# Performance work log

Measured on AMD Instinct MI355X. Metric: run time of the kernel, lower is better.

## Reference

```python
import jax, jax.numpy as jnp
import numpy as np

BATCH, FIELD0, EMB = 1024, 32, 64
LAYER_SIZES = (128, 128, 128)  # split_half=True -> hidden field sizes [32, 64, 64]


def setup_inputs() -> dict:
    key = jax.random.key(0)
    ks = jax.random.split(key, 7)
    x = jax.random.normal(ks[0], (BATCH, FIELD0, EMB), dtype=jnp.float32)
    # Conv1D(kernel_size=1) weights: (in_channels=f0*fi, filters=layer_size), plus bias.
    field_sizes = [FIELD0]
    params = {}
    for i, size in enumerate(LAYER_SIZES):
        fi = field_sizes[-1]
        fan_in = FIELD0 * fi
        scale = 1.0 / np.sqrt(fan_in)
        params[f"W{i}"] = jax.random.normal(ks[1 + 2 * i], (fan_in, size), dtype=jnp.float32) * scale
        params[f"b{i}"] = jnp.zeros((size,), dtype=jnp.float32)
        field_sizes.append(size // 2 if i != len(LAYER_SIZES) - 1 else size)
    return {"x": x, **params}


def reference(x, W0, b0, W1, b1, W2, b2):
    # CIN: outer product + 1x1 conv (a matmul over the flattened field-pair axis)
    # fused as a single bilinear contraction per layer:
    #   cur[b,k,e] = sum_{i,j} x[b,i,e] * hidden[b,j,e] * W[i,j,k] + b[k]
    Ws = [(W0, b0), (W1, b1), (W2, b2)]
    f0 = x.shape[1]
    hidden = x
    final_outputs = []
    n_layers = len(Ws)
    for idx, (W, b) in enumerate(Ws):
        fi = hidden.shape[1]
        Wr = W.reshape(f0, fi, W.shape[-1])  # channel m = i*fi + j (row-major reshape)
        cur = jnp.einsum('bie,bje,ijk->bke', x, hidden, Wr) + b[None, :, None]
        # activation=None -> linear
        if idx != n_layers - 1:
            half = cur.shape[1] // 2
            hidden, direct = cur[:, :half, :], cur[:, half:, :]
        else:
            direct = cur
        final_outputs.append(direct)
    result = jnp.concatenate(final_outputs, axis=1)  # (B, 64+64+128, E)
    return jnp.sum(result, axis=-1)  # (B, 256)
```

## Files before the change

kernel.cpp:

```cpp
#include <hip/hip_runtime.h>
#include <cstdint>


typedef _Float16 half8  __attribute__((ext_vector_type(8)));
typedef _Float16 half4_ __attribute__((ext_vector_type(4)));
typedef _Float16 half2_ __attribute__((ext_vector_type(2)));
typedef float    f32x4  __attribute__((ext_vector_type(4)));

__global__ void pack_w_all(const float* __restrict__ W0, _Float16* __restrict__ Wt0,
                           const float* __restrict__ W1, _Float16* __restrict__ Wt1,
                           const float* __restrict__ W2, _Float16* __restrict__ Wt2)
{
    __shared__ _Float16 ldsT[128 * 33];
    const int blk = blockIdx.x, t = threadIdx.x;
    const float* W;
    _Float16* Wt;
    int c;
    if (blk < 32)       { W = W0; Wt = Wt0; c = blk; }
    else if (blk < 96)  { W = W1; Wt = Wt1; c = blk - 32; }
    else                { W = W2; Wt = Wt2; c = blk - 96; }

    for (int p = t; p < 32 * 128; p += 256) {
        int kk = p >> 7, m = p & 127;
        ldsT[m * 33 + kk] = (_Float16)W[(size_t)(c * 32 + kk) * 128 + m];
    }
    __syncthreads();
    int m = t >> 1, kk0 = (t & 1) * 16;
    half8 v0, v1;
#pragma unroll
    for (int i = 0; i < 8; ++i) {
        v0[i] = ldsT[m * 33 + kk0 + i];
        v1[i] = ldsT[m * 33 + kk0 + 8 + i];
    }
    *(half8*)(Wt + (size_t)c * 4096 + t * 16)     = v0;
    *(half8*)(Wt + (size_t)c * 4096 + t * 16 + 8) = v1;
}

template<int NCH, int ISH, int PH>
__device__ __forceinline__ void kloop_t(f32x4 (&acc)[2][4],
    const _Float16* __restrict__ WtL, const _Float16* __restrict__ hb,
    const _Float16* __restrict__ sX, int lr, int q, int ms, int kh)
{
#pragma unroll
    for (int mt = 0; mt < 2; ++mt)
#pragma unroll
        for (int nt = 0; nt < 4; ++nt)
            acc[mt][nt] = f32x4{0.0f, 0.0f, 0.0f, 0.0f};

    constexpr int HC = NCH / 2;
    const int c0 = kh * HC;
    const _Float16* aG = WtL + (size_t)c0 * 4096 + (ms * 32 + lr) * 32 + q * 8;
    const _Float16* hP = hb + lr * PH + q * 8;
    const _Float16* xP = sX + lr;

    half8 afA[2], afB[2], hvA[4], hvB[4];
    _Float16 xsA[4], xsB[4];

    auto pf = [&](half8* af, half8* hv, _Float16* xs, int cc) {
        const int c  = c0 + cc;
        const int i  = c >> ISH;
        const int j0 = (c & ((1 << ISH) - 1)) << 5;
        const _Float16* ag = aG + (size_t)cc * 4096;
        af[0] = *(const half8*)(ag);
        af[1] = *(const half8*)(ag + 512);
        const _Float16* hh = hP + j0;
        const _Float16* xb = xP + (i << 6);
#pragma unroll
        for (int nt = 0; nt < 4; ++nt) {
            hv[nt] = *(const half8*)(hh + nt * (PH * 16));
            xs[nt] = xb[nt * 16];
        }
    };
    auto cp = [&](half8* af, half8* hv, _Float16* xs) {
#pragma unroll
        for (int nt = 0; nt < 4; ++nt) {
            half2_ xv2 = {xs[nt], xs[nt]};
            half8 xv8 = __builtin_shufflevector(xv2, xv2, 0, 1, 0, 1, 0, 1, 0, 1);
            half8 bf = hv[nt] * xv8;
            acc[0][nt] = __builtin_amdgcn_mfma_f32_16x16x32_f16(
                af[0], bf, acc[0][nt], 0, 0, 0);
            acc[1][nt] = __builtin_amdgcn_mfma_f32_16x16x32_f16(
                af[1], bf, acc[1][nt], 0, 0, 0);
        }
    };

    pf(afA, hvA, xsA, 0);
    for (int cc = 0; cc < HC; cc += 2) {
        pf(afB, hvB, xsB, cc + 1);
        cp(afA, hvA, xsA);
        if (cc + 2 < HC) pf(afA, hvA, xsA, cc + 2);
        cp(afB, hvB, xsB);
    }
}

__global__ __launch_bounds__(256, 2)
void cin_fused(const float* __restrict__ x,
               const _Float16* __restrict__ Wt0,
               const _Float16* __restrict__ Wt1,
               const float* __restrict__ bs0,
               const float* __restrict__ bs1,
               _Float16* __restrict__ S0,
               _Float16* __restrict__ S1,
               _Float16* __restrict__ S2)
{
    __shared__ alignas(16) char smem[38912];
    _Float16* sX  = (_Float16*)smem;
    _Float16* R_A = (_Float16*)(smem + 4096);
    _Float16* R_B = (_Float16*)(smem + 13312);
    f32x4*    XC  = (f32x4*)   (smem + 22528);

    const int t = threadIdx.x, lane = t & 63, w = t >> 6;
    const int ms = w >> 1, kh = w & 1;
    const int lr = lane & 15, q = lane >> 4;
    const int b = blockIdx.x;

    {
        const float4* xv = (const float4*)(x + (size_t)b * 2048);
#pragma unroll
        for (int s = 0; s < 2; ++s) {
            int p4 = t + s * 256;
            float4 v = xv[p4];
            int idx = p4 * 4, i = idx >> 6, e0 = idx & 63;
            _Float16 h0 = (_Float16)v.x, h1 = (_Float16)v.y;
            _Float16 h2 = (_Float16)v.z, h3 = (_Float16)v.w;
            half4_ pk = {h0, h1, h2, h3};
            *(half4_*)(sX + i * 64 + e0) = pk;
            *(half4_*)(R_B + i * 72 + e0) = pk;
            R_A[(e0 + 0) * 40 + i] = h0;
            R_A[(e0 + 1) * 40 + i] = h1;
            R_A[(e0 + 2) * 40 + i] = h2;
            R_A[(e0 + 3) * 40 + i] = h3;
        }
    }
    __syncthreads();

    half8 aF[2][2];
#pragma unroll
    for (int it = 0; it < 2; ++it) {
        aF[it][0] = *(const half8*)(R_B + (it * 16 + lr) * 72 + q * 8);
        aF[it][1] = *(const half8*)(R_B + (it * 16 + lr) * 72 + q * 8 + 32);
    }

    f32x4 acc[2][4];

    const int wslot = ms * 2 + kh, pslot = ms * 2 + (1 - kh);
    auto xw = [&](const f32x4 (&a)[4]) {
#pragma unroll
        for (int nt = 0; nt < 4; ++nt)
            XC[wslot * 256 + nt * 64 + lane] = a[nt];
    };
    auto xr = [&](f32x4 (&a)[4]) {
#pragma unroll
        for (int nt = 0; nt < 4; ++nt)
            a[nt] += XC[pslot * 256 + nt * 64 + lane];
    };

    auto sgemm = [&](const _Float16* hJ, int fi, _Float16* Sdst) {
        const int nT = fi >> 3;
        for (int tt = w; tt < nT; tt += 4) {
            const int it = tt & 1, jt = tt >> 1;
            f32x4 sa = {0.0f, 0.0f, 0.0f, 0.0f};
            half8 bv0 = *(const half8*)(hJ + (jt * 16 + lr) * 72 + q * 8);
            half8 bv1 = *(const half8*)(hJ + (jt * 16 + lr) * 72 + q * 8 + 32);
            sa = __builtin_amdgcn_mfma_f32_16x16x32_f16(aF[it][0], bv0, sa, 0, 0, 0);
            sa = __builtin_amdgcn_mfma_f32_16x16x32_f16(aF[it][1], bv1, sa, 0, 0, 0);
#pragma unroll
            for (int r = 0; r < 4; ++r)
                Sdst[(size_t)b * (32 * fi) + (it * 16 + q * 4 + r) * fi
                     + jt * 16 + lr] = (_Float16)sa[r];
        }
    };

    auto epi_rows = [&](const f32x4 (&a)[4], const float* bs,
                        _Float16* hJ, _Float16* hT, bool wantT) {
        const int jb = ms * 32 + kh * 16 + q * 4;
        const float b0f = bs[jb + 0], b1f = bs[jb + 1];
        const float b2f = bs[jb + 2], b3f = bs[jb + 3];
#pragma unroll
        for (int nt = 0; nt < 4; ++nt) {
            const int e = nt * 16 + lr;
            half4_ vh;
            vh[0] = (_Float16)(a[nt][0] + b0f);
            vh[1] = (_Float16)(a[nt][1] + b1f);
            vh[2] = (_Float16)(a[nt][2] + b2f);
            vh[3] = (_Float16)(a[nt][3] + b3f);
            hJ[(jb + 0) * 72 + e] = vh[0];
            hJ[(jb + 1) * 72 + e] = vh[1];
            hJ[(jb + 2) * 72 + e] = vh[2];
            hJ[(jb + 3) * 72 + e] = vh[3];
            if (wantT) *(half4_*)(hT + e * 72 + jb) = vh;
        }
    };
    auto combine_epi = [&](const float* bs, _Float16* hJ, _Float16* hT,
                           bool wantT) {
        if (kh == 0) { xr(acc[0]); epi_rows(acc[0], bs, hJ, hT, wantT); }
        else         { xr(acc[1]); epi_rows(acc[1], bs, hJ, hT, wantT); }
    };

    sgemm(R_B, 32, S0);
    kloop_t<32, 0, 40>(acc, Wt0, R_A, sX, lr, q, ms, kh);
    if (kh == 0) xw(acc[1]); else xw(acc[0]);
    __syncthreads();
    combine_epi(bs0, R_A, R_B, true);
    __syncthreads();
    sgemm(R_A, 64, S1);
    kloop_t<64, 1, 72>(acc, Wt1, R_B, sX, lr, q, ms, kh);
    if (kh == 0) xw(acc[1]); else xw(acc[0]);
    __syncthreads();
    combine_epi(bs1, R_B, nullptr, false);
    __syncthreads();
    sgemm(R_B, 64, S2);
}

__global__ __launch_bounds__(256, 4)
void cin_direct(const _Float16* __restrict__ S0v, const _Float16* __restrict__ S1v,
                const _Float16* __restrict__ S2v,
                const _Float16* __restrict__ Wt0, const _Float16* __restrict__ Wt1,
                const _Float16* __restrict__ Wt2,
                const float* __restrict__ bs0, const float* __restrict__ bs1,
                const float* __restrict__ bs2,
                float* __restrict__ out)
{
    __shared__ f32x4 red[3][64];
    const int t = threadIdx.x, lane = t & 63, kh = t >> 6;
    const int lr = lane & 15, q = lane >> 4;
    const int task = blockIdx.x;

    const _Float16 *S, *Wt;
    const float* bias;
    int fan, nch, dm0, ob, idx;
    if (task < 256)      { S = S0v; Wt = Wt0; bias = bs0; fan = 1024; nch = 32; dm0 = 64; ob = 0;   idx = task; }
    else if (task < 512) { S = S1v; Wt = Wt1; bias = bs1; fan = 2048; nch = 64; dm0 = 64; ob = 64;  idx = task - 256; }
    else                 { S = S2v; Wt = Wt2; bias = bs2; fan = 2048; nch = 64; dm0 = 0;  ob = 128; idx = task - 512; }
    const int bt = idx & 63, kt = idx >> 6;
    const int bbase = bt * 16;
    const int hq = nch >> 2, c0 = kh * hq;

    const _Float16* aG = Wt + (size_t)(dm0 + kt * 16 + lr) * 32 + q * 8
                            + (size_t)c0 * 4096;
    const _Float16* bG = S + (size_t)(bbase + lr) * fan + q * 8 + c0 * 32;

    f32x4 acc = {0.0f, 0.0f, 0.0f, 0.0f};
    half8 aA = *(const half8*)(aG);
    half8 bA = *(const half8*)(bG);
    for (int c = 0; c < hq; c += 2) {
        half8 aB = *(const half8*)(aG + (size_t)(c + 1) * 4096);
        half8 bB = *(const half8*)(bG + (c + 1) * 32);
        acc = __builtin_amdgcn_mfma_f32_16x16x32_f16(aA, bA, acc, 0, 0, 0);
        if (c + 2 < hq) {
            aA = *(const half8*)(aG + (size_t)(c + 2) * 4096);
            bA = *(const half8*)(bG + (c + 2) * 32);
        }
        acc = __builtin_amdgcn_mfma_f32_16x16x32_f16(aB, bB, acc, 0, 0, 0);
    }
    if (kh != 0) red[kh - 1][lane] = acc;
    __syncthreads();
    if (kh == 0) {
#pragma unroll
        for (int p = 0; p < 3; ++p) {
            f32x4 o = red[p][lane];
#pragma unroll
            for (int r = 0; r < 4; ++r) acc[r] += o[r];
        }
#pragma unroll
        for (int r = 0; r < 4; ++r) {
            int kl = kt * 16 + q * 4 + r;
            out[(size_t)(bbase + lr) * 256 + ob + kl]
                = acc[r] + 64.0f * bias[dm0 + kl];
        }
    }
}

extern "C" void kernel_launch(void* const* d_in, const int* in_sizes, int n_in,
                              void* d_out, int out_size, void* d_ws, size_t ws_size,
                              hipStream_t stream)
{
    const float* x  = (const float*)d_in[0];
    const float* W0 = (const float*)d_in[1];
    const float* b0 = (const float*)d_in[2];
    const float* W1 = (const float*)d_in[3];
    const float* b1 = (const float*)d_in[4];
    const float* W2 = (const float*)d_in[5];
    const float* b2 = (const float*)d_in[6];
    float* out = (float*)d_out;

    char* ws = (char*)d_ws;
    _Float16* Wt0 = (_Float16*)(ws + 0);
    _Float16* Wt1 = (_Float16*)(ws + 262144);
    _Float16* Wt2 = (_Float16*)(ws + 786432);
    _Float16* S0  = (_Float16*)(ws + 1310720);
    _Float16* S1  = (_Float16*)(ws + 3407872);
    _Float16* S2  = (_Float16*)(ws + 7602176);
    (void)in_sizes; (void)n_in; (void)out_size; (void)ws_size;

    hipLaunchKernelGGL(pack_w_all, dim3(160), dim3(256), 0, stream,
                       W0, Wt0, W1, Wt1, W2, Wt2);

    hipLaunchKernelGGL(cin_fused, dim3(1024), dim3(256), 0, stream,
                       x, Wt0, Wt1, b0, b1, S0, S1, S2);

    hipLaunchKernelGGL(cin_direct, dim3(1024), dim3(256), 0, stream,
                       S0, S1, S2, Wt0, Wt1, Wt2, b0, b1, b2, out);
}
```

Baseline: 140.9 us.

## Split K four ways across waves and exchange partial sums in fp16 LDS

Result: faster. 115.5 us (-18.0%).

```diff
diff --git a/kernel.cpp b/kernel.cpp
--- a/kernel.cpp
+++ b/kernel.cpp
@@ -37,23 +37,23 @@
 }
 
 template<int NCH, int ISH, int PH>
-__device__ __forceinline__ void kloop_t(f32x4 (&acc)[2][4],
+__device__ __forceinline__ void kloop_t(f32x4 (&acc)[4][4],
     const _Float16* __restrict__ WtL, const _Float16* __restrict__ hb,
-    const _Float16* __restrict__ sX, int lr, int q, int ms, int kh)
-{
-#pragma unroll
-    for (int mt = 0; mt < 2; ++mt)
+    const _Float16* __restrict__ sX, int lr, int q, int w)
+{
+#pragma unroll
+    for (int mt = 0; mt < 4; ++mt)
 #pragma unroll
         for (int nt = 0; nt < 4; ++nt)
             acc[mt][nt] = f32x4{0.0f, 0.0f, 0.0f, 0.0f};
 
-    constexpr int HC = NCH / 2;
-    const int c0 = kh * HC;
-    const _Float16* aG = WtL + (size_t)c0 * 4096 + (ms * 32 + lr) * 32 + q * 8;
+    constexpr int HC = NCH / 4;
+    const int c0 = w * HC;
+    const _Float16* aG = WtL + (size_t)c0 * 4096 + lr * 32 + q * 8;
     const _Float16* hP = hb + lr * PH + q * 8;
     const _Float16* xP = sX + lr;
 
-    half8 afA[2], afB[2], hvA[4], hvB[4];
+    half8 afA[4], afB[4], hvA[4], hvB[4];
     _Float16 xsA[4], xsB[4];
 
     auto pf = [&](half8* af, half8* hv, _Float16* xs, int cc) {
@@ -61,8 +61,9 @@
         const int i  = c >> ISH;
         const int j0 = (c & ((1 << ISH) - 1)) << 5;
         const _Float16* ag = aG + (size_t)cc * 4096;
-        af[0] = *(const half8*)(ag);
-        af[1] = *(const half8*)(ag + 512);
+#pragma unroll
+        for (int mt = 0; mt < 4; ++mt)
+            af[mt] = *(const half8*)(ag + mt * 512);
         const _Float16* hh = hP + j0;
         const _Float16* xb = xP + (i << 6);
 #pragma unroll
@@ -77,10 +78,10 @@
             half2_ xv2 = {xs[nt], xs[nt]};
             half8 xv8 = __builtin_shufflevector(xv2, xv2, 0, 1, 0, 1, 0, 1, 0, 1);
             half8 bf = hv[nt] * xv8;
-            acc[0][nt] = __builtin_amdgcn_mfma_f32_16x16x32_f16(
-                af[0], bf, acc[0][nt], 0, 0, 0);
-            acc[1][nt] = __builtin_amdgcn_mfma_f32_16x16x32_f16(
-                af[1], bf, acc[1][nt], 0, 0, 0);
+#pragma unroll
+            for (int mt = 0; mt < 4; ++mt)
+                acc[mt][nt] = __builtin_amdgcn_mfma_f32_16x16x32_f16(
+                    af[mt], bf, acc[mt][nt], 0, 0, 0);
         }
     };
 
@@ -103,14 +104,13 @@
                _Float16* __restrict__ S1,
                _Float16* __restrict__ S2)
 {
-    __shared__ alignas(16) char smem[38912];
-    _Float16* sX  = (_Float16*)smem;
-    _Float16* R_A = (_Float16*)(smem + 4096);
-    _Float16* R_B = (_Float16*)(smem + 13312);
-    f32x4*    XC  = (f32x4*)   (smem + 22528);
+    __shared__ alignas(16) char smem[47104];
+    _Float16* sX   = (_Float16*)smem;
+    _Float16* R_A  = (_Float16*)(smem + 4096);
+    _Float16* R_B  = (_Float16*)(smem + 13312);
+    _Float16* XC16 = (_Float16*)(smem + 22528);
 
     const int t = threadIdx.x, lane = t & 63, w = t >> 6;
-    const int ms = w >> 1, kh = w & 1;
     const int lr = lane & 15, q = lane >> 4;
     const int b = blockIdx.x;
 
@@ -134,56 +134,56 @@
     }
     __syncthreads();
 
-    half8 aF[2][2];
-#pragma unroll
-    for (int it = 0; it < 2; ++it) {
-        aF[it][0] = *(const half8*)(R_B + (it * 16 + lr) * 72 + q * 8);
-        aF[it][1] = *(const half8*)(R_B + (it * 16 + lr) * 72 + q * 8 + 32);
-    }
-
-    f32x4 acc[2][4];
-
-    const int wslot = ms * 2 + kh, pslot = ms * 2 + (1 - kh);
-    auto xw = [&](const f32x4 (&a)[4]) {
-#pragma unroll
-        for (int nt = 0; nt < 4; ++nt)
-            XC[wslot * 256 + nt * 64 + lane] = a[nt];
-    };
-    auto xr = [&](f32x4 (&a)[4]) {
-#pragma unroll
-        for (int nt = 0; nt < 4; ++nt)
-            a[nt] += XC[pslot * 256 + nt * 64 + lane];
-    };
-
-    auto sgemm = [&](const _Float16* hJ, int fi, _Float16* Sdst) {
-        const int nT = fi >> 3;
-        for (int tt = w; tt < nT; tt += 4) {
-            const int it = tt & 1, jt = tt >> 1;
-            f32x4 sa = {0.0f, 0.0f, 0.0f, 0.0f};
-            half8 bv0 = *(const half8*)(hJ + (jt * 16 + lr) * 72 + q * 8);
-            half8 bv1 = *(const half8*)(hJ + (jt * 16 + lr) * 72 + q * 8 + 32);
-            sa = __builtin_amdgcn_mfma_f32_16x16x32_f16(aF[it][0], bv0, sa, 0, 0, 0);
-            sa = __builtin_amdgcn_mfma_f32_16x16x32_f16(aF[it][1], bv1, sa, 0, 0, 0);
-#pragma unroll
-            for (int r = 0; r < 4; ++r)
-                Sdst[(size_t)b * (32 * fi) + (it * 16 + q * 4 + r) * fi
-                     + jt * 16 + lr] = (_Float16)sa[r];
-        }
-    };
-
-    auto epi_rows = [&](const f32x4 (&a)[4], const float* bs,
-                        _Float16* hJ, _Float16* hT, bool wantT) {
-        const int jb = ms * 32 + kh * 16 + q * 4;
+    const int it = w & 1;
+    const half8 aF0 = *(const half8*)(R_B + (it * 16 + lr) * 72 + q * 8);
+    const half8 aF1 = *(const half8*)(R_B + (it * 16 + lr) * 72 + q * 8 + 32);
+
+    f32x4 acc[4][4];
+
+    auto xchg_write = [&]() {
+#pragma unroll
+        for (int mt = 0; mt < 4; ++mt) {
+            if (mt == w) continue;
+            const int slot = mt * 3 + (w > mt ? w - 1 : w);
+#pragma unroll
+            for (int cc = 0; cc < 2; ++cc) {
+                half8 hv8;
+#pragma unroll
+                for (int r = 0; r < 4; ++r) {
+                    hv8[r]     = (_Float16)acc[mt][cc * 2][r];
+                    hv8[4 + r] = (_Float16)acc[mt][cc * 2 + 1][r];
+                }
+                *(half8*)(XC16 + slot * 1024 + cc * 512 + lane * 8) = hv8;
+            }
+        }
+    };
+
+    auto finish = [&](f32x4 (&aw)[4], const float* bs,
+                      _Float16* hJ, _Float16* hT, bool wantT) {
+#pragma unroll
+        for (int p = 0; p < 3; ++p) {
+#pragma unroll
+            for (int cc = 0; cc < 2; ++cc) {
+                half8 hv8 = *(const half8*)(XC16 + (w * 3 + p) * 1024
+                                            + cc * 512 + lane * 8);
+#pragma unroll
+                for (int r = 0; r < 4; ++r) {
+                    aw[cc * 2][r]     += (float)hv8[r];
+                    aw[cc * 2 + 1][r] += (float)hv8[4 + r];
+                }
+            }
+        }
+        const int jb = w * 16 + q * 4;
         const float b0f = bs[jb + 0], b1f = bs[jb + 1];
         const float b2f = bs[jb + 2], b3f = bs[jb + 3];
 #pragma unroll
         for (int nt = 0; nt < 4; ++nt) {
             const int e = nt * 16 + lr;
             half4_ vh;
-            vh[0] = (_Float16)(a[nt][0] + b0f);
-            vh[1] = (_Float16)(a[nt][1] + b1f);
-            vh[2] = (_Float16)(a[nt][2] + b2f);
-            vh[3] = (_Float16)(a[nt][3] + b3f);
+            vh[0] = (_Float16)(aw[nt][0] + b0f);
+            vh[1] = (_Float16)(aw[nt][1] + b1f);
+            vh[2] = (_Float16)(aw[nt][2] + b2f);
+            vh[3] = (_Float16)(aw[nt][3] + b3f);
             hJ[(jb + 0) * 72 + e] = vh[0];
             hJ[(jb + 1) * 72 + e] = vh[1];
             hJ[(jb + 2) * 72 + e] = vh[2];
@@ -193,23 +193,41 @@
     };
     auto combine_epi = [&](const float* bs, _Float16* hJ, _Float16* hT,
                            bool wantT) {
-        if (kh == 0) { xr(acc[0]); epi_rows(acc[0], bs, hJ, hT, wantT); }
-        else         { xr(acc[1]); epi_rows(acc[1], bs, hJ, hT, wantT); }
+        if (w == 0)      finish(acc[0], bs, hJ, hT, wantT);
+        else if (w == 1) finish(acc[1], bs, hJ, hT, wantT);
+        else if (w == 2) finish(acc[2], bs, hJ, hT, wantT);
+        else             finish(acc[3], bs, hJ, hT, wantT);
+    };
+
+    auto sgemm = [&](const _Float16* hJ, int fi, _Float16* Sdst) {
+        const int nT = fi >> 3;
+        for (int tt = w; tt < nT; tt += 4) {
+            const int jt = tt >> 1;
+            f32x4 sa = {0.0f, 0.0f, 0.0f, 0.0f};
+            half8 bv0 = *(const half8*)(hJ + (jt * 16 + lr) * 72 + q * 8);
+            half8 bv1 = *(const half8*)(hJ + (jt * 16 + lr) * 72 + q * 8 + 32);
+            sa = __builtin_amdgcn_mfma_f32_16x16x32_f16(aF0, bv0, sa, 0, 0, 0);
+            sa = __builtin_amdgcn_mfma_f32_16x16x32_f16(aF1, bv1, sa, 0, 0, 0);
+#pragma unroll
+            for (int r = 0; r < 4; ++r)
+                Sdst[(size_t)b * (32 * fi) + (it * 16 + q * 4 + r) * fi
+                     + jt * 16 + lr] = (_Float16)sa[r];
+        }
     };
 
     sgemm(R_B, 32, S0);
-    kloop_t<32, 0, 40>(acc, Wt0, R_A, sX, lr, q, ms, kh);
-    if (kh == 0) xw(acc[1]); else xw(acc[0]);
+    kloop_t<32, 0, 40>(acc, Wt0, R_A, sX, lr, q, w);
+    xchg_write();
     __syncthreads();
     combine_epi(bs0, R_A, R_B, true);
     __syncthreads();
     sgemm(R_A, 64, S1);
-    kloop_t<64, 1, 72>(acc, Wt1, R_B, sX, lr, q, ms, kh);
-    if (kh == 0) xw(acc[1]); else xw(acc[0]);
-    __syncthreads();
-    combine_epi(bs1, R_B, nullptr, false);
-    __syncthreads();
-    sgemm(R_B, 64, S2);
+    kloop_t<64, 1, 72>(acc, Wt1, R_B, sX, lr, q, w);
+    xchg_write();
+    __syncthreads();
+    combine_epi(bs1, R_A, nullptr, false);
+    __syncthreads();
+    sgemm(R_A, 64, S2);
 }
 
 __global__ __launch_bounds__(256, 4)
```

## Assign one batch per wavefront in fused CIN kernel, reorder weight packing

Applied to the files above, without the earlier changes.

Measured after the change: 123.8 us. -12.2%, faster.

```diff
diff --git a/kernel.cpp b/kernel.cpp
--- a/kernel.cpp
+++ b/kernel.cpp
@@ -15,14 +15,14 @@
     const int blk = blockIdx.x, t = threadIdx.x;
     const float* W;
     _Float16* Wt;
-    int c;
-    if (blk < 32)       { W = W0; Wt = Wt0; c = blk; }
-    else if (blk < 96)  { W = W1; Wt = Wt1; c = blk - 32; }
-    else                { W = W2; Wt = Wt2; c = blk - 96; }
+    int c, fi;
+    if (blk < 32)       { W = W0; Wt = Wt0; c = blk;      fi = 32; }
+    else if (blk < 96)  { W = W1; Wt = Wt1; c = blk - 32; fi = 64; }
+    else                { W = W2; Wt = Wt2; c = blk - 96; fi = 64; }
 
     for (int p = t; p < 32 * 128; p += 256) {
         int kk = p >> 7, m = p & 127;
-        ldsT[m * 33 + kk] = (_Float16)W[(size_t)(c * 32 + kk) * 128 + m];
+        ldsT[m * 33 + kk] = (_Float16)W[(size_t)(kk * fi + c) * 128 + m];
     }
     __syncthreads();
     int m = t >> 1, kk0 = (t & 1) * 16;
@@ -36,60 +36,52 @@
     *(half8*)(Wt + (size_t)c * 4096 + t * 16 + 8) = v1;
 }
 
-template<int NCH, int ISH, int PH>
-__device__ __forceinline__ void kloop_t(f32x4 (&acc)[2][4],
-    const _Float16* __restrict__ WtL, const _Float16* __restrict__ hb,
-    const _Float16* __restrict__ sX, int lr, int q, int ms, int kh)
-{
-#pragma unroll
-    for (int mt = 0; mt < 2; ++mt)
+template<int NCH>
+__device__ __forceinline__ void kloop_t(f32x4 (&acc)[4][4],
+    const _Float16* __restrict__ WtL, const _Float16* __restrict__ hB,
+    const half8 (&xF)[4], int lr, int q)
+{
+#pragma unroll
+    for (int mt = 0; mt < 4; ++mt)
 #pragma unroll
         for (int nt = 0; nt < 4; ++nt)
             acc[mt][nt] = f32x4{0.0f, 0.0f, 0.0f, 0.0f};
 
-    constexpr int HC = NCH / 2;
-    const int c0 = kh * HC;
-    const _Float16* aG = WtL + (size_t)c0 * 4096 + (ms * 32 + lr) * 32 + q * 8;
-    const _Float16* hP = hb + lr * PH + q * 8;
-    const _Float16* xP = sX + lr;
-
-    half8 afA[2], afB[2], hvA[4], hvB[4];
+    const _Float16* aG = WtL + lr * 32 + q * 8;
+
+    half8 afA[4], afB[4];
     _Float16 xsA[4], xsB[4];
 
-    auto pf = [&](half8* af, half8* hv, _Float16* xs, int cc) {
-        const int c  = c0 + cc;
-        const int i  = c >> ISH;
-        const int j0 = (c & ((1 << ISH) - 1)) << 5;
+    auto pf = [&](half8* af, _Float16* xs, int cc) {
         const _Float16* ag = aG + (size_t)cc * 4096;
-        af[0] = *(const half8*)(ag);
-        af[1] = *(const half8*)(ag + 512);
-        const _Float16* hh = hP + j0;
-        const _Float16* xb = xP + (i << 6);
-#pragma unroll
-        for (int nt = 0; nt < 4; ++nt) {
-            hv[nt] = *(const half8*)(hh + nt * (PH * 16));
-            xs[nt] = xb[nt * 16];
-        }
-    };
-    auto cp = [&](half8* af, half8* hv, _Float16* xs) {
+#pragma unroll
+        for (int mt = 0; mt < 4; ++mt)
+            af[mt] = *(const half8*)(ag + mt * 512);
+#pragma unroll
+        for (int nt = 0; nt < 4; ++nt)
+            xs[nt] = hB[cc * 72 + nt * 16 + lr];
+    };
+    auto cp = [&](half8* af, _Float16* xs) {
+        __builtin_amdgcn_s_setprio(1);
 #pragma unroll
         for (int nt = 0; nt < 4; ++nt) {
             half2_ xv2 = {xs[nt], xs[nt]};
             half8 xv8 = __builtin_shufflevector(xv2, xv2, 0, 1, 0, 1, 0, 1, 0, 1);
-            half8 bf = hv[nt] * xv8;
-            acc[0][nt] = __builtin_amdgcn_mfma_f32_16x16x32_f16(
-                af[0], bf, acc[0][nt], 0, 0, 0);
-            acc[1][nt] = __builtin_amdgcn_mfma_f32_16x16x32_f16(
-                af[1], bf, acc[1][nt], 0, 0, 0);
-        }
-    };
-
-    pf(afA, hvA, xsA, 0);
-    for (int cc = 0; cc < HC; cc += 2) {
-        pf(afB, hvB, xsB, cc + 1);
-        cp(afA, hvA, xsA);
-        if (cc + 2 < HC) pf(afA, hvA, xsA, cc + 2);
-        cp(afB, hvB, xsB);
+            half8 bf = xF[nt] * xv8;
+#pragma unroll
+            for (int mt = 0; mt < 4; ++mt)
+                acc[mt][nt] = __builtin_amdgcn_mfma_f32_16x16x32_f16(
+                    af[mt], bf, acc[mt][nt], 0, 0, 0);
+        }
+        __builtin_amdgcn_s_setprio(0);
+    };
+
+    pf(afA, xsA, 0);
+    for (int cc = 0; cc < NCH; cc += 2) {
+        pf(afB, xsB, cc + 1);
+        cp(afA, xsA);
+        if (cc + 2 < NCH) pf(afA, xsA, cc + 2);
+        cp(afB, xsB);
     }
 }
 
@@ -103,116 +95,90 @@
                _Float16* __restrict__ S1,
                _Float16* __restrict__ S2)
 {
-    __shared__ alignas(16) char smem[38912];
-    _Float16* sX  = (_Float16*)smem;
-    _Float16* R_A = (_Float16*)(smem + 4096);
-    _Float16* R_B = (_Float16*)(smem + 13312);
-    f32x4*    XC  = (f32x4*)   (smem + 22528);
-
+    __shared__ alignas(16) char smem[57344];
     const int t = threadIdx.x, lane = t & 63, w = t >> 6;
-    const int ms = w >> 1, kh = w & 1;
     const int lr = lane & 15, q = lane >> 4;
-    const int b = blockIdx.x;
+    const int batch = blockIdx.x * 4 + w;
+
+    _Float16* hB = (_Float16*)(smem + w * 14336);
+    _Float16* xT = (_Float16*)(smem + w * 14336 + 9216);
 
     {
-        const float4* xv = (const float4*)(x + (size_t)b * 2048);
-#pragma unroll
-        for (int s = 0; s < 2; ++s) {
-            int p4 = t + s * 256;
+        const float4* xv = (const float4*)(x + (size_t)batch * 2048);
+#pragma unroll
+        for (int s = 0; s < 8; ++s) {
+            int p4 = lane + s * 64;
             float4 v = xv[p4];
             int idx = p4 * 4, i = idx >> 6, e0 = idx & 63;
             _Float16 h0 = (_Float16)v.x, h1 = (_Float16)v.y;
             _Float16 h2 = (_Float16)v.z, h3 = (_Float16)v.w;
             half4_ pk = {h0, h1, h2, h3};
-            *(half4_*)(sX + i * 64 + e0) = pk;
-            *(half4_*)(R_B + i * 72 + e0) = pk;
-            R_A[(e0 + 0) * 40 + i] = h0;
-            R_A[(e0 + 1) * 40 + i] = h1;
-            R_A[(e0 + 2) * 40 + i] = h2;
-            R_A[(e0 + 3) * 40 + i] = h3;
-        }
-    }
-    __syncthreads();
-
-    half8 aF[2][2];
-#pragma unroll
-    for (int it = 0; it < 2; ++it) {
-        aF[it][0] = *(const half8*)(R_B + (it * 16 + lr) * 72 + q * 8);
-        aF[it][1] = *(const half8*)(R_B + (it * 16 + lr) * 72 + q * 8 + 32);
-    }
-
-    f32x4 acc[2][4];
-
-    const int wslot = ms * 2 + kh, pslot = ms * 2 + (1 - kh);
-    auto xw = [&](const f32x4 (&a)[4]) {
-#pragma unroll
-        for (int nt = 0; nt < 4; ++nt)
-            XC[wslot * 256 + nt * 64 + lane] = a[nt];
-    };
-    auto xr = [&](f32x4 (&a)[4]) {
-#pragma unroll
-        for (int nt = 0; nt < 4; ++nt)
-            a[nt] += XC[pslot * 256 + nt * 64 + lane];
-    };
-
-    auto sgemm = [&](const _Float16* hJ, int fi, _Float16* Sdst) {
-        const int nT = fi >> 3;
-        for (int tt = w; tt < nT; tt += 4) {
-            const int it = tt & 1, jt = tt >> 1;
+            *(half4_*)(hB + i * 72 + e0) = pk;
+            xT[(e0 + 0) * 40 + i] = h0;
+            xT[(e0 + 1) * 40 + i] = h1;
+            xT[(e0 + 2) * 40 + i] = h2;
+            xT[(e0 + 3) * 40 + i] = h3;
+        }
+    }
+
+    half8 xF[4];
+#pragma unroll
+    for (int nt = 0; nt < 4; ++nt)
+        xF[nt] = *(const half8*)(xT + (nt * 16 + lr) * 40 + q * 8);
+    const half8 aF00 = *(const half8*)(hB + lr * 72 + q * 8);
+    const half8 aF01 = *(const half8*)(hB + lr * 72 + q * 8 + 32);
+    const half8 aF10 = *(const half8*)(hB + (16 + lr) * 72 + q * 8);
+    const half8 aF11 = *(const half8*)(hB + (16 + lr) * 72 + q * 8 + 32);
+
+    f32x4 acc[4][4];
+
+    auto epi = [&](const float* bs) {
+#pragma unroll
+        for (int mt = 0; mt < 4; ++mt) {
+            const int jb = mt * 16 + q * 4;
+            const float b0f = bs[jb + 0], b1f = bs[jb + 1];
+            const float b2f = bs[jb + 2], b3f = bs[jb + 3];
+#pragma unroll
+            for (int nt = 0; nt < 4; ++nt) {
+                const int e = nt * 16 + lr;
+                hB[(jb + 0) * 72 + e] = (_Float16)(acc[mt][nt][0] + b0f);
+                hB[(jb + 1) * 72 + e] = (_Float16)(acc[mt][nt][1] + b1f);
+                hB[(jb + 2) * 72 + e] = (_Float16)(acc[mt][nt][2] + b2f);
+                hB[(jb + 3) * 72 + e] = (_Float16)(acc[mt][nt][3] + b3f);
+            }
+        }
+    };
+
+    auto sgemm = [&](int fi, _Float16* Sdst) {
+        const int njt = fi >> 4;
+        _Float16* Sb = Sdst + (size_t)batch * (32 * fi);
+        for (int jt = 0; jt < njt; ++jt) {
+            half8 bv0 = *(const half8*)(hB + (jt * 16 + lr) * 72 + q * 8);
+            half8 bv1 = *(const half8*)(hB + (jt * 16 + lr) * 72 + q * 8 + 32);
             f32x4 sa = {0.0f, 0.0f, 0.0f, 0.0f};
-            half8 bv0 = *(const half8*)(hJ + (jt * 16 + lr) * 72 + q * 8);
-            half8 bv1 = *(const half8*)(hJ + (jt * 16 + lr) * 72 + q * 8 + 32);
-            sa = __builtin_amdgcn_mfma_f32_16x16x32_f16(aF[it][0], bv0, sa, 0, 0, 0);
-            sa = __builtin_amdgcn_mfma_f32_16x16x32_f16(aF[it][1], bv1, sa, 0, 0, 0);
-#pragma unroll
-            for (int r = 0; r < 4; ++r)
-                Sdst[(size_t)b * (32 * fi) + (it * 16 + q * 4 + r) * fi
-                     + jt * 16 + lr] = (_Float16)sa[r];
-        }
-    };
-
-    auto epi_rows = [&](const f32x4 (&a)[4], const float* bs,
-                        _Float16* hJ, _Float16* hT, bool wantT) {
-        const int jb = ms * 32 + kh * 16 + q * 4;
-        const float b0f = bs[jb + 0], b1f = bs[jb + 1];
-        const float b2f = bs[jb + 2], b3f = bs[jb + 3];
-#pragma unroll
-        for (int nt = 0; nt < 4; ++nt) {
-            const int e = nt * 16 + lr;
-            half4_ vh;
-            vh[0] = (_Float16)(a[nt][0] + b0f);
-            vh[1] = (_Float16)(a[nt][1] + b1f);
-            vh[2] = (_Float16)(a[nt][2] + b2f);
-            vh[3] = (_Float16)(a[nt][3] + b3f);
-            hJ[(jb + 0) * 72 + e] = vh[0];
-            hJ[(jb + 1) * 72 + e] = vh[1];
-            hJ[(jb + 2) * 72 + e] = vh[2];
-            hJ[(jb + 3) * 72 + e] = vh[3];
-            if (wantT) *(half4_*)(hT + e * 72 + jb) = vh;
-        }
-    };
-    auto combine_epi = [&](const float* bs, _Float16* hJ, _Float16* hT,
-                           bool wantT) {
-        if (kh == 0) { xr(acc[0]); epi_rows(acc[0], bs, hJ, hT, wantT); }
-        else         { xr(acc[1]); epi_rows(acc[1], bs, hJ, hT, wantT); }
-    };
-
-    sgemm(R_B, 32, S0);
-    kloop_t<32, 0, 40>(acc, Wt0, R_A, sX, lr, q, ms, kh);
-    if (kh == 0) xw(acc[1]); else xw(acc[0]);
-    __syncthreads();
-    combine_epi(bs0, R_A, R_B, true);
-    __syncthreads();
-    sgemm(R_A, 64, S1);
-    kloop_t<64, 1, 72>(acc, Wt1, R_B, sX, lr, q, ms, kh);
-    if (kh == 0) xw(acc[1]); else xw(acc[0]);
-    __syncthreads();
-    combine_epi(bs1, R_B, nullptr, false);
-    __syncthreads();
-    sgemm(R_B, 64, S2);
-}
-
-__global__ __launch_bounds__(256, 4)
+            sa = __builtin_amdgcn_mfma_f32_16x16x32_f16(aF00, bv0, sa, 0, 0, 0);
+            sa = __builtin_amdgcn_mfma_f32_16x16x32_f16(aF01, bv1, sa, 0, 0, 0);
+            f32x4 sb = {0.0f, 0.0f, 0.0f, 0.0f};
+            sb = __builtin_amdgcn_mfma_f32_16x16x32_f16(aF10, bv0, sb, 0, 0, 0);
+            sb = __builtin_amdgcn_mfma_f32_16x16x32_f16(aF11, bv1, sb, 0, 0, 0);
+            half4_ v0, v1;
+#pragma unroll
+            for (int r = 0; r < 4; ++r) { v0[r] = (_Float16)sa[r]; v1[r] = (_Float16)sb[r]; }
+            *(half4_*)(Sb + (jt * 16 + lr) * 32 + q * 4)      = v0;
+            *(half4_*)(Sb + (jt * 16 + lr) * 32 + 16 + q * 4) = v1;
+        }
+    };
+
+    sgemm(32, S0);
+    kloop_t<32>(acc, Wt0, hB, xF, lr, q);
+    epi(bs0);
+    sgemm(64, S1);
+    kloop_t<64>(acc, Wt1, hB, xF, lr, q);
+    epi(bs1);
+    sgemm(64, S2);
+}
+
+__global__ __launch_bounds__(256, 2)
 void cin_direct(const _Float16* __restrict__ S0v, const _Float16* __restrict__ S1v,
                 const _Float16* __restrict__ S2v,
                 const _Float16* __restrict__ Wt0, const _Float16* __restrict__ Wt1,
@@ -296,7 +262,7 @@
     hipLaunchKernelGGL(pack_w_all, dim3(160), dim3(256), 0, stream,
                        W0, Wt0, W1, Wt1, W2, Wt2);
 
-    hipLaunchKernelGGL(cin_fused, dim3(1024), dim3(256), 0, stream,
+    hipLaunchKernelGGL(cin_fused, dim3(256), dim3(256), 0, stream,
                        x, Wt0, Wt1, b0, b1, S0, S1, S2);
 
     hipLaunchKernelGGL(cin_direct, dim3(1024), dim3(256), 0, stream,
```
